# Performance work log

Hardware: AMD Instinct MI355X
Metric: run time of the kernel (lower is better)

Reference implementation:

```python
import jax, jax.numpy as jnp
import numpy as np

N, E, IN_C, DIM, OUT_C, G = 40000, 640000, 128, 128, 16, 256
BN_EPS = 1e-5

def setup_inputs() -> dict:
    key = jax.random.key(0)
    ks = jax.random.split(key, 24)
    x = jax.random.normal(ks[0], (N, IN_C), dtype=jnp.float32)
    edge_index = jax.random.randint(ks[1], (2, E), 0, N, dtype=jnp.int32)
    batch = jnp.sort(jax.random.randint(ks[2], (N,), 0, G, dtype=jnp.int32))
    s = 1.0 / np.sqrt(DIM)
    # layer 1 (in_channels -> dim)
    W1_0 = jax.random.uniform(ks[3], (IN_C, DIM), jnp.float32, -s, s)
    b1_0 = jnp.zeros((DIM,), jnp.float32)
    g_0 = jnp.ones((DIM,), jnp.float32)
    bt_0 = jnp.zeros((DIM,), jnp.float32)
    W2_0 = jax.random.uniform(ks[4], (DIM, DIM), jnp.float32, -s, s)
    b2_0 = jnp.zeros((DIM,), jnp.float32)
    # layers 2-5 stacked (dim -> dim)
    W1s = jax.random.uniform(ks[5], (4, DIM, DIM), jnp.float32, -s, s)
    b1s = jnp.zeros((4, DIM), jnp.float32)
    gs = jnp.ones((4, DIM), jnp.float32)
    bts = jnp.zeros((4, DIM), jnp.float32)
    W2s = jax.random.uniform(ks[6], (4, DIM, DIM), jnp.float32, -s, s)
    b2s = jnp.zeros((4, DIM), jnp.float32)
    lin1_W = jax.random.uniform(ks[7], (DIM, DIM), jnp.float32, -s, s)
    lin1_b = jnp.zeros((DIM,), jnp.float32)
    lin2_W = jax.random.uniform(ks[8], (DIM, OUT_C), jnp.float32, -s, s)
    lin2_b = jnp.zeros((OUT_C,), jnp.float32)
    return dict(x=x, edge_index=edge_index, batch=batch, num_graphs=G,
                W1_0=W1_0, b1_0=b1_0, g_0=g_0, bt_0=bt_0, W2_0=W2_0, b2_0=b2_0,
                W1s=W1s, b1s=b1s, gs=gs, bts=bts, W2s=W2s, b2s=b2s,
                lin1_W=lin1_W, lin1_b=lin1_b, lin2_W=lin2_W, lin2_b=lin2_b)

def _gin_layer(x, src, dst, W1, b1, g, bt, W2, b2):
    # GIN aggregation: (1 + eps) * x_i + sum_{j in N(i)} x_j, eps = 0
    agg = jax.ops.segment_sum(x[src], dst, num_segments=x.shape[0])
    h = (x + agg) @ W1 + b1
    # BatchNorm1d over nodes (training-mode batch stats, biased variance)
    mu = h.mean(axis=0)
    var = h.var(axis=0)
    h = (h - mu) * jax.lax.rsqrt(var + BN_EPS) * g + bt
    h = jax.nn.relu(h)
    return jax.nn.relu(h @ W2 + b2)

def reference(x, edge_index, batch, num_graphs,
              W1_0, b1_0, g_0, bt_0, W2_0, b2_0,
              W1s, b1s, gs, bts, W2s, b2s,
              lin1_W, lin1_b, lin2_W, lin2_b):
    src, dst = edge_index[0], edge_index[1]
    h = _gin_layer(x, src, dst, W1_0, b1_0, g_0, bt_0, W2_0, b2_0)
    for i in range(4):
        h = _gin_layer(h, src, dst, W1s[i], b1s[i], gs[i], bts[i], W2s[i], b2s[i])
    x1 = h  # dropout p=0.2 in eval mode = identity
    pooled = jax.ops.segment_sum(x1, batch, num_segments=num_graphs)  # [G, DIM]
    out = jax.nn.relu(pooled @ lin1_W + lin1_b)
    out = out @ lin2_W + lin2_b
    return (jax.nn.log_softmax(out, axis=-1), x1)
```

## Files before the change

### kernel.cpp

```cpp
#include <hip/hip_runtime.h>

namespace {

constexpr int N    = 40000;
constexpr int E    = 640000;
constexpr int DIM  = 128;
constexpr int NG   = 256;
constexpr int OUTC = 16;
constexpr int STRIDE = 48;
constexpr float BN_EPS = 1e-5f;

typedef __attribute__((ext_vector_type(8))) short bf16x8;
typedef __attribute__((ext_vector_type(4))) float f32x4;
typedef __attribute__((ext_vector_type(2))) float f32x2;

__device__ __forceinline__ void atomAddF(float* p, float v) {
  unsafeAtomicAdd(p, v);
}

__device__ __forceinline__ unsigned b16r(float f) {
  unsigned u = __float_as_uint(f);
  return (u + 0x7fffu + ((u >> 16) & 1u)) >> 16;
}
__device__ __forceinline__ unsigned pack2(float a, float b) {
  return b16r(a) | (b16r(b) << 16);
}

__device__ __forceinline__ unsigned pk4_fp8(float4 v) {
  unsigned u = __builtin_amdgcn_cvt_pk_fp8_f32(v.x, v.y, 0, false);
  u = __builtin_amdgcn_cvt_pk_fp8_f32(v.z, v.w, u, true);
  return u;
}
__device__ __forceinline__ void addfp8x4(float* a, unsigned u) {
  f32x2 lo = __builtin_amdgcn_cvt_pk_f32_fp8(u, false);
  f32x2 hi = __builtin_amdgcn_cvt_pk_f32_fp8(u, true);
  a[0] += lo[0]; a[1] += lo[1]; a[2] += hi[0]; a[3] += hi[1];
}
__device__ __forceinline__ void add16(float* a, const uint4 v) {
  addfp8x4(a, v.x); addfp8x4(a + 4, v.y); addfp8x4(a + 8, v.z); addfp8x4(a + 12, v.w);
}

__device__ __forceinline__ int rot4(int r) {
  return ((r << 1) | ((r >> 3) & 1)) & 15;
}

__device__ __forceinline__ bf16x8 bnrelu8(bf16x8 a, const float* sc, const float* sh) {
  union { bf16x8 v; unsigned u[4]; } in, out;
  in.v = a;
#pragma unroll
  for (int p = 0; p < 4; ++p) {
    float lo = __uint_as_float(in.u[p] << 16);
    float hi = __uint_as_float(in.u[p] & 0xffff0000u);
    lo = fmaxf(fmaf(lo, sc[2 * p], sh[2 * p]), 0.f);
    hi = fmaxf(fmaf(hi, sc[2 * p + 1], sh[2 * p + 1]), 0.f);
    out.u[p] = pack2(lo, hi);
  }
  return out.v;
}

constexpr int CVT_B   = (N * DIM / 4) / 256;
constexpr int FILL_B  = E / 256;
constexpr int TRANS_B = 10 * DIM / 4;

__global__ __launch_bounds__(256) void prep_kernel(const float* __restrict__ x,
                                                   unsigned char* __restrict__ xf8,
                                                   const int* __restrict__ src,
                                                   const int* __restrict__ dst,
                                                   int* __restrict__ cnt,
                                                   int* __restrict__ col,
                                                   const float* __restrict__ W1_0,
                                                   const float* __restrict__ W2_0,
                                                   const float* __restrict__ W1s,
                                                   const float* __restrict__ W2s,
                                                   ushort* __restrict__ Wt) {
  const int b = blockIdx.x;
  if (b < CVT_B) {
    const int i = b * 256 + threadIdx.x;
    float4 v = ((const float4*)x)[i];
    ((unsigned*)xf8)[i] = pk4_fp8(v);
  } else if (b < CVT_B + FILL_B) {
    const int e = (b - CVT_B) * 256 + threadIdx.x;
    const int d = dst[e];
    int p = atomicAdd(&cnt[d], 1);
    if (p < STRIDE) col[d * STRIDE + p] = src[e];
  } else {
    const int ob   = (b - CVT_B - FILL_B) * 4 + (threadIdx.x >> 6);
    const int lane = threadIdx.x & 63;
    const int m = ob >> 7;
    const int c = ob & 127;
    const int l = m >> 1;
    const float* W;
    if (l == 0) W = (m & 1) ? W2_0 : W1_0;
    else        W = ((m & 1) ? W2s : W1s) + (size_t)(l - 1) * DIM * DIM;
    const int k = lane * 2;
    float f0 = W[(size_t)k * DIM + c];
    float f1 = W[(size_t)(k + 1) * DIM + c];
    ((unsigned*)Wt)[((size_t)m * DIM + c) * 64 + lane] = pack2(f0, f1);
  }
}


__global__ __launch_bounds__(256) void gin1_fused(const unsigned char* __restrict__ xf8,
                                                  const int* __restrict__ cnt,
                                                  const int* __restrict__ col,
                                                  const ushort* __restrict__ Wt1,
                                                  const float* __restrict__ b1,
                                                  ushort* __restrict__ h,
                                                  float* __restrict__ stats8) {
  __shared__ uint4 tile4[32 * 16];
  const int tid   = threadIdx.x;
  const int node0 = blockIdx.x * 32;

  {
    const int r = tid >> 3;
    const int l = tid & 7;
    const int node = node0 + r;
    const uint4* __restrict__ x16 = (const uint4*)xf8;
    float a[16];
#pragma unroll
    for (int i = 0; i < 16; ++i) a[i] = 0.f;
    add16(a, x16[(size_t)node * 8 + l]);
    int n = cnt[node];
    n = (n < STRIDE) ? n : STRIDE;
    const int base = node * STRIDE;
    int k = 0;
    for (; k + 4 <= n; k += 4) {
      int j0 = col[base + k], j1 = col[base + k + 1];
      int j2 = col[base + k + 2], j3 = col[base + k + 3];
      uint4 v0 = x16[(size_t)j0 * 8 + l];
      uint4 v1 = x16[(size_t)j1 * 8 + l];
      uint4 v2 = x16[(size_t)j2 * 8 + l];
      uint4 v3 = x16[(size_t)j3 * 8 + l];
      add16(a, v0); add16(a, v1); add16(a, v2); add16(a, v3);
    }
    for (; k < n; ++k) add16(a, x16[(size_t)col[base + k] * 8 + l]);
    uint4 o0 = {pack2(a[0], a[1]), pack2(a[2], a[3]), pack2(a[4], a[5]), pack2(a[6], a[7])};
    uint4 o1 = {pack2(a[8], a[9]), pack2(a[10], a[11]), pack2(a[12], a[13]), pack2(a[14], a[15])};
    const int sw = rot4(r & 15);
    tile4[r * 16 + ((2 * l) ^ sw)]     = o0;
    tile4[r * 16 + ((2 * l + 1) ^ sw)] = o1;
  }
  __syncthreads();

  const int lane = tid & 63;
  const int c0   = __builtin_amdgcn_readfirstlane((tid >> 6) * 32);
  const int lr   = lane & 15;
  const int lg   = lane >> 4;

  const bf16x8* __restrict__ tb = (const bf16x8*)tile4;
  const int r0 = lr, r1 = lr + 16;
  const int sw0 = rot4(lr);

  const ushort* __restrict__ brow = Wt1 + (size_t)(c0 + lr) * DIM + lg * 8;

  f32x4 acc[2][2];
#pragma unroll
  for (int i = 0; i < 2; ++i)
#pragma unroll
    for (int j = 0; j < 2; ++j) acc[i][j] = {0, 0, 0, 0};

#pragma unroll
  for (int ks = 0; ks < 4; ++ks) {
    bf16x8 a0 = tb[r0 * 16 + ((lg + ks * 4) ^ sw0)];
    bf16x8 a1 = tb[r1 * 16 + ((lg + ks * 4) ^ sw0)];
    bf16x8 b0 = *(const bf16x8*)(brow + ks * 32);
    bf16x8 b1v = *(const bf16x8*)(brow + 16 * DIM + ks * 32);
    acc[0][0] = __builtin_amdgcn_mfma_f32_16x16x32_bf16(a0, b0, acc[0][0], 0, 0, 0);
    acc[0][1] = __builtin_amdgcn_mfma_f32_16x16x32_bf16(a0, b1v, acc[0][1], 0, 0, 0);
    acc[1][0] = __builtin_amdgcn_mfma_f32_16x16x32_bf16(a1, b0, acc[1][0], 0, 0, 0);
    acc[1][1] = __builtin_amdgcn_mfma_f32_16x16x32_bf16(a1, b1v, acc[1][1], 0, 0, 0);
  }

  float s[2] = {0, 0}, q[2] = {0, 0};
#pragma unroll
  for (int rf = 0; rf < 2; ++rf) {
#pragma unroll
    for (int cf = 0; cf < 2; ++cf) {
      const int colidx = c0 + cf * 16 + lr;
      const float bb = b1[colidx];
#pragma unroll
      for (int rg = 0; rg < 4; ++rg) {
        float v = acc[rf][cf][rg] + bb;
        const int row = node0 + rf * 16 + lg * 4 + rg;
        __builtin_nontemporal_store((ushort)b16r(v), &h[(size_t)row * DIM + colidx]);
        s[cf] += v; q[cf] = fmaf(v, v, q[cf]);
      }
    }
  }
#pragma unroll
  for (int cf = 0; cf < 2; ++cf) {
    float ss = s[cf], qq = q[cf];
    ss += __shfl_xor(ss, 16); ss += __shfl_xor(ss, 32);
    qq += __shfl_xor(qq, 16); qq += __shfl_xor(qq, 32);
    if (lg == 0) {
      float* st = stats8 + (blockIdx.x & 7) * 2 * DIM;
      atomAddF(&st[c0 + cf * 16 + lr], ss);
      atomAddF(&st[DIM + c0 + cf * 16 + lr], qq);
    }
  }
}


template <int F32OUT>
__global__ __launch_bounds__(256) void gin2_fused(const ushort* __restrict__ h,
                                                  const float* __restrict__ stats8,
                                                  const float* __restrict__ gamma,
                                                  const float* __restrict__ beta,
                                                  const ushort* __restrict__ Wt2,
                                                  const float* __restrict__ b2,
                                                  unsigned char* __restrict__ xf8,
                                                  float* __restrict__ outf) {
  __shared__ float lsc[DIM], lsh[DIM];
  const int tid = threadIdx.x;
  if (tid < DIM) {
    float s = 0.f, q = 0.f;
#pragma unroll
    for (int p = 0; p < 8; ++p) {
      s += stats8[p * 2 * DIM + tid];
      q += stats8[p * 2 * DIM + DIM + tid];
    }
    const float inv_n = 1.0f / N;
    float mu  = s * inv_n;
    float var = q * inv_n - mu * mu;
    float sc  = gamma[tid] * rsqrtf(var + BN_EPS);
    lsc[tid] = sc;
    lsh[tid] = beta[tid] - mu * sc;
  }
  __syncthreads();

  const int lane = tid & 63;
  const int c0   = __builtin_amdgcn_readfirstlane((tid >> 6) * 32);
  const int lr   = lane & 15;
  const int lg   = lane >> 4;
  const int row0 = blockIdx.x * 32;

  const ushort* __restrict__ arow = h + (size_t)(row0 + lr) * DIM + lg * 8;
  const ushort* __restrict__ brow = Wt2 + (size_t)(c0 + lr) * DIM + lg * 8;

  f32x4 acc00 = {0, 0, 0, 0}, acc01 = {0, 0, 0, 0}, acc10 = {0, 0, 0, 0}, acc11 = {0, 0, 0, 0};

#pragma unroll
  for (int ks = 0; ks < 4; ++ks) {
    const int ch0 = lg * 8 + ks * 32;
    float sc[8], sh[8];
    *(float4*)(sc)     = *(const float4*)&lsc[ch0];
    *(float4*)(sc + 4) = *(const float4*)&lsc[ch0 + 4];
    *(float4*)(sh)     = *(const float4*)&lsh[ch0];
    *(float4*)(sh + 4) = *(const float4*)&lsh[ch0 + 4];
    bf16x8 ra0 = __builtin_nontemporal_load((const bf16x8*)(arow + ks * 32));
    bf16x8 ra1 = __builtin_nontemporal_load((const bf16x8*)(arow + 16 * DIM + ks * 32));
    bf16x8 a0 = bnrelu8(ra0, sc, sh);
    bf16x8 a1 = bnrelu8(ra1, sc, sh);
    bf16x8 b0 = *(const bf16x8*)(brow + ks * 32);
    bf16x8 b1 = *(const bf16x8*)(brow + 16 * DIM + ks * 32);
    acc00 = __builtin_amdgcn_mfma_f32_16x16x32_bf16(a0, b0, acc00, 0, 0, 0);
    acc01 = __builtin_amdgcn_mfma_f32_16x16x32_bf16(a0, b1, acc01, 0, 0, 0);
    acc10 = __builtin_amdgcn_mfma_f32_16x16x32_bf16(a1, b0, acc10, 0, 0, 0);
    acc11 = __builtin_amdgcn_mfma_f32_16x16x32_bf16(a1, b1, acc11, 0, 0, 0);
  }

  const float bia0 = b2[c0 + lr];
  const float bia1 = b2[c0 + 16 + lr];
  f32x4 accs[2][2] = {{acc00, acc01}, {acc10, acc11}};
#pragma unroll
  for (int rf = 0; rf < 2; ++rf) {
#pragma unroll
    for (int cf = 0; cf < 2; ++cf) {
      const int colidx = c0 + cf * 16 + lr;
      const float bb = cf ? bia1 : bia0;
#pragma unroll
      for (int rg = 0; rg < 4; ++rg) {
        float v = fmaxf(accs[rf][cf][rg] + bb, 0.f);
        const int row = row0 + rf * 16 + lg * 4 + rg;
        if (F32OUT) {
          __builtin_nontemporal_store(v, &outf[(size_t)row * DIM + colidx]);
        } else {
          float vp = __shfl_xor(v, 1);
          if (!(lr & 1)) {
            unsigned pk = __builtin_amdgcn_cvt_pk_fp8_f32(v, vp, 0, false);
            *(ushort*)(xf8 + (size_t)row * DIM + colidx) = (ushort)pk;
          }
        }
      }
    }
  }
}


__global__ __launch_bounds__(256) void pool_kernel(const float* __restrict__ x1,
                                                   const int* __restrict__ batch,
                                                   float* __restrict__ pooled) {
  const int grp  = (blockIdx.x * blockDim.x + threadIdx.x) >> 5;
  const int lane = threadIdx.x & 31;
  const int node0 = grp * 64;
  if (node0 >= N) return;
  const int end = (node0 + 64 < N) ? (node0 + 64) : N;
  float4 acc = {0, 0, 0, 0};
  int cur = batch[node0];
  for (int n = node0; n < end; ++n) {
    int b = batch[n];
    if (b != cur) {
      atomAddF(&pooled[(size_t)cur * DIM + lane * 4 + 0], acc.x);
      atomAddF(&pooled[(size_t)cur * DIM + lane * 4 + 1], acc.y);
      atomAddF(&pooled[(size_t)cur * DIM + lane * 4 + 2], acc.z);
      atomAddF(&pooled[(size_t)cur * DIM + lane * 4 + 3], acc.w);
      acc = {0, 0, 0, 0};
      cur = b;
    }
    f32x4 v = __builtin_nontemporal_load((const f32x4*)x1 + (size_t)n * 32 + lane);
    acc.x += v[0]; acc.y += v[1]; acc.z += v[2]; acc.w += v[3];
  }
  atomAddF(&pooled[(size_t)cur * DIM + lane * 4 + 0], acc.x);
  atomAddF(&pooled[(size_t)cur * DIM + lane * 4 + 1], acc.y);
  atomAddF(&pooled[(size_t)cur * DIM + lane * 4 + 2], acc.z);
  atomAddF(&pooled[(size_t)cur * DIM + lane * 4 + 3], acc.w);
}


__global__ __launch_bounds__(128) void mlp_kernel(const float* __restrict__ pooled,
                                                  const float* __restrict__ W1,
                                                  const float* __restrict__ b1,
                                                  const float* __restrict__ W2,
                                                  const float* __restrict__ b2,
                                                  float* __restrict__ out) {
  const int gidx = blockIdx.x;
  const int t    = threadIdx.x;
  __shared__ float p[DIM], a1[DIM];
  p[t] = pooled[(size_t)gidx * DIM + t];
  __syncthreads();
  float acc = b1[t];
  for (int k = 0; k < DIM; ++k) acc = fmaf(p[k], W1[(size_t)k * DIM + t], acc);
  a1[t] = fmaxf(acc, 0.f);
  __syncthreads();
  if (t < OUTC) {
    float o = b2[t];
    for (int k = 0; k < DIM; ++k) o = fmaf(a1[k], W2[(size_t)k * OUTC + t], o);
    float m = o;
    for (int s = 8; s >= 1; s >>= 1) m = fmaxf(m, __shfl_xor(m, s, 16));
    float e = __expf(o - m);
    float se = e;
    for (int s = 8; s >= 1; s >>= 1) se += __shfl_xor(se, s, 16);
    out[(size_t)gidx * OUTC + t] = o - m - __logf(se);
  }
}

}

extern "C" void kernel_launch(void* const* d_in, const int* in_sizes, int n_in,
                              void* d_out, int out_size, void* d_ws, size_t ws_size,
                              hipStream_t stream) {
  const float* x     = (const float*)d_in[0];
  const int*   ei    = (const int*)d_in[1];
  const int*   batch = (const int*)d_in[2];
  const float* W1_0  = (const float*)d_in[4];
  const float* b1_0  = (const float*)d_in[5];
  const float* g_0   = (const float*)d_in[6];
  const float* bt_0  = (const float*)d_in[7];
  const float* W2_0  = (const float*)d_in[8];
  const float* b2_0  = (const float*)d_in[9];
  const float* W1s   = (const float*)d_in[10];
  const float* b1s   = (const float*)d_in[11];
  const float* gs    = (const float*)d_in[12];
  const float* bts   = (const float*)d_in[13];
  const float* W2s   = (const float*)d_in[14];
  const float* b2s   = (const float*)d_in[15];
  const float* lin1W = (const float*)d_in[16];
  const float* lin1b = (const float*)d_in[17];
  const float* lin2W = (const float*)d_in[18];
  const float* lin2b = (const float*)d_in[19];

  float* out_ls = (float*)d_out;
  float* x1_out = (float*)d_out + NG * OUTC;

  char* w = (char*)d_ws;
  auto alloc = [&](size_t bytes) -> void* {
    void* p = (void*)w;
    w += (bytes + 255) & ~(size_t)255;
    return p;
  };
  int*    cnt      = (int*)alloc((size_t)N * 4);
  float*  statsAll = (float*)alloc((size_t)(5 * 8 * 2 * DIM + NG * DIM) * 4);
  float*  pooled   = statsAll + 5 * 8 * 2 * DIM;
  const size_t zero_bytes = (size_t)((N * 4 + 255) & ~255) +
                            (size_t)(5 * 8 * 2 * DIM + NG * DIM) * 4;

  int*    col    = (int*)alloc((size_t)N * STRIDE * 4);
  unsigned char* xf8 = (unsigned char*)alloc((size_t)N * DIM);
  ushort* act    = (ushort*)alloc((size_t)N * DIM * 2);
  ushort* Wt     = (ushort*)alloc((size_t)10 * DIM * DIM * 2);

  const int* src = ei;
  const int* dst = ei + E;

  (void)hipMemsetAsync(cnt, 0, zero_bytes, stream);

  prep_kernel<<<CVT_B + FILL_B + TRANS_B, 256, 0, stream>>>(x, xf8, src, dst, cnt, col,
                                                            W1_0, W2_0, W1s, W2s, Wt);

  for (int l = 0; l < 5; ++l) {
    const float* b1 = (l == 0) ? b1_0 : b1s + (size_t)(l - 1) * DIM;
    const float* gg = (l == 0) ? g_0  : gs  + (size_t)(l - 1) * DIM;
    const float* bb = (l == 0) ? bt_0 : bts + (size_t)(l - 1) * DIM;
    const float* b2 = (l == 0) ? b2_0 : b2s + (size_t)(l - 1) * DIM;
    const ushort* Wt1 = Wt + (size_t)(2 * l) * DIM * DIM;
    const ushort* Wt2 = Wt + (size_t)(2 * l + 1) * DIM * DIM;
    float* stats8 = statsAll + (size_t)l * 8 * 2 * DIM;

    gin1_fused<<<N / 32, 256, 0, stream>>>(xf8, cnt, col, Wt1, b1, act, stats8);
    if (l == 4)
      gin2_fused<1><<<N / 32, 256, 0, stream>>>(act, stats8, gg, bb, Wt2, b2, nullptr, x1_out);
    else
      gin2_fused<0><<<N / 32, 256, 0, stream>>>(act, stats8, gg, bb, Wt2, b2, xf8, nullptr);
  }

  {
    int groups = (N + 63) / 64;
    int blocks = (groups * 32 + 255) / 256;
    pool_kernel<<<blocks, 256, 0, stream>>>(x1_out, batch, pooled);
  }
  mlp_kernel<<<NG, 128, 0, stream>>>(pooled, lin1W, lin1b, lin2W, lin2b, out_ls);
}
```

Measured before the change: 321.7 us.

## Fuse graph pooling into last GIN layer, compact CSR indices, drop memset

Removes the separate pool kernel by doing segmented per-graph sums with atomics in the epilogue of the final gin2 kernel, so x1 is not read back. Replaces hipMemsetAsync with zeroing blocks inside prep_kernel and splits the CSR fill into its own kernel, which is needed because zeroing must finish before the count atomics. Column indices are stored as ushort to halve adjacency traffic. Nontemporal hints on the h store and load are dropped so the intermediate can stay in cache. Risks: ushort indices only hold values below 65536 (N=40000 fits), more atomics on pooled, and one extra kernel launch.

```diff
diff --git a/kernel.cpp b/kernel.cpp
--- a/kernel.cpp
+++ b/kernel.cpp
@@ -59,32 +59,27 @@
 }
 
 constexpr int CVT_B   = (N * DIM / 4) / 256;
-constexpr int FILL_B  = E / 256;
 constexpr int TRANS_B = 10 * DIM / 4;
+constexpr size_t ZERO_BYTES = (size_t)((N * 4 + 255) & ~255) +
+                              (size_t)(5 * 8 * 2 * DIM) * 4 +
+                              (size_t)(NG * DIM) * 4;
+constexpr int ZERO_B  = (int)((ZERO_BYTES / 16 + 255) / 256);
 
 __global__ __launch_bounds__(256) void prep_kernel(const float* __restrict__ x,
                                                    unsigned char* __restrict__ xf8,
-                                                   const int* __restrict__ src,
-                                                   const int* __restrict__ dst,
-                                                   int* __restrict__ cnt,
-                                                   int* __restrict__ col,
                                                    const float* __restrict__ W1_0,
                                                    const float* __restrict__ W2_0,
                                                    const float* __restrict__ W1s,
                                                    const float* __restrict__ W2s,
-                                                   ushort* __restrict__ Wt) {
+                                                   ushort* __restrict__ Wt,
+                                                   uint4* __restrict__ zp) {
   const int b = blockIdx.x;
   if (b < CVT_B) {
     const int i = b * 256 + threadIdx.x;
     float4 v = ((const float4*)x)[i];
     ((unsigned*)xf8)[i] = pk4_fp8(v);
-  } else if (b < CVT_B + FILL_B) {
-    const int e = (b - CVT_B) * 256 + threadIdx.x;
-    const int d = dst[e];
-    int p = atomicAdd(&cnt[d], 1);
-    if (p < STRIDE) col[d * STRIDE + p] = src[e];
-  } else {
-    const int ob   = (b - CVT_B - FILL_B) * 4 + (threadIdx.x >> 6);
+  } else if (b < CVT_B + TRANS_B) {
+    const int ob   = (b - CVT_B) * 4 + (threadIdx.x >> 6);
     const int lane = threadIdx.x & 63;
     const int m = ob >> 7;
     const int c = ob & 127;
@@ -96,13 +91,27 @@
     float f0 = W[(size_t)k * DIM + c];
     float f1 = W[(size_t)(k + 1) * DIM + c];
     ((unsigned*)Wt)[((size_t)m * DIM + c) * 64 + lane] = pack2(f0, f1);
-  }
+  } else {
+    const size_t i = (size_t)(b - CVT_B - TRANS_B) * 256 + threadIdx.x;
+    if (i * 16 < ZERO_BYTES) zp[i] = {0, 0, 0, 0};
+  }
+}
+
+
+__global__ __launch_bounds__(256) void fill_kernel(const int* __restrict__ src,
+                                                   const int* __restrict__ dst,
+                                                   int* __restrict__ cnt,
+                                                   ushort* __restrict__ col) {
+  const int e = blockIdx.x * 256 + threadIdx.x;
+  const int d = dst[e];
+  int p = atomicAdd(&cnt[d], 1);
+  if (p < STRIDE) col[d * STRIDE + p] = (ushort)src[e];
 }
 
 
 __global__ __launch_bounds__(256) void gin1_fused(const unsigned char* __restrict__ xf8,
                                                   const int* __restrict__ cnt,
-                                                  const int* __restrict__ col,
+                                                  const ushort* __restrict__ col,
                                                   const ushort* __restrict__ Wt1,
                                                   const float* __restrict__ b1,
                                                   ushort* __restrict__ h,
@@ -182,7 +191,7 @@
       for (int rg = 0; rg < 4; ++rg) {
         float v = acc[rf][cf][rg] + bb;
         const int row = node0 + rf * 16 + lg * 4 + rg;
-        __builtin_nontemporal_store((ushort)b16r(v), &h[(size_t)row * DIM + colidx]);
+        h[(size_t)row * DIM + colidx] = (ushort)b16r(v);
         s[cf] += v; q[cf] = fmaf(v, v, q[cf]);
       }
     }
@@ -209,7 +218,9 @@
                                                   const ushort* __restrict__ Wt2,
                                                   const float* __restrict__ b2,
                                                   unsigned char* __restrict__ xf8,
-                                                  float* __restrict__ outf) {
+                                                  float* __restrict__ outf,
+                                                  const int* __restrict__ batch,
+                                                  float* __restrict__ pooled) {
   __shared__ float lsc[DIM], lsh[DIM];
   const int tid = threadIdx.x;
   if (tid < DIM) {
@@ -247,10 +258,8 @@
     *(float4*)(sc + 4) = *(const float4*)&lsc[ch0 + 4];
     *(float4*)(sh)     = *(const float4*)&lsh[ch0];
     *(float4*)(sh + 4) = *(const float4*)&lsh[ch0 + 4];
-    bf16x8 ra0 = __builtin_nontemporal_load((const bf16x8*)(arow + ks * 32));
-    bf16x8 ra1 = __builtin_nontemporal_load((const bf16x8*)(arow + 16 * DIM + ks * 32));
-    bf16x8 a0 = bnrelu8(ra0, sc, sh);
-    bf16x8 a1 = bnrelu8(ra1, sc, sh);
+    bf16x8 a0 = bnrelu8(*(const bf16x8*)(arow + ks * 32), sc, sh);
+    bf16x8 a1 = bnrelu8(*(const bf16x8*)(arow + 16 * DIM + ks * 32), sc, sh);
     bf16x8 b0 = *(const bf16x8*)(brow + ks * 32);
     bf16x8 b1 = *(const bf16x8*)(brow + 16 * DIM + ks * 32);
     acc00 = __builtin_amdgcn_mfma_f32_16x16x32_bf16(a0, b0, acc00, 0, 0, 0);
@@ -262,19 +271,44 @@
   const float bia0 = b2[c0 + lr];
   const float bia1 = b2[c0 + 16 + lr];
   f32x4 accs[2][2] = {{acc00, acc01}, {acc10, acc11}};
-#pragma unroll
-  for (int rf = 0; rf < 2; ++rf) {
-#pragma unroll
-    for (int cf = 0; cf < 2; ++cf) {
-      const int colidx = c0 + cf * 16 + lr;
-      const float bb = cf ? bia1 : bia0;
-#pragma unroll
-      for (int rg = 0; rg < 4; ++rg) {
-        float v = fmaxf(accs[rf][cf][rg] + bb, 0.f);
-        const int row = row0 + rf * 16 + lg * 4 + rg;
-        if (F32OUT) {
-          __builtin_nontemporal_store(v, &outf[(size_t)row * DIM + colidx]);
-        } else {
+
+  if (F32OUT) {
+    const int rbase = row0 + lg * 4;
+#pragma unroll
+    for (int rf = 0; rf < 2; ++rf) {
+      const int r0_ = rbase + rf * 16;
+      int4 b4 = *(const int4*)&batch[r0_];
+      const int bb_[4] = {b4.x, b4.y, b4.z, b4.w};
+#pragma unroll
+      for (int cf = 0; cf < 2; ++cf) {
+        const int colidx = c0 + cf * 16 + lr;
+        const float bia = cf ? bia1 : bia0;
+        float run = 0.f;
+        int cur = bb_[0];
+#pragma unroll
+        for (int rg = 0; rg < 4; ++rg) {
+          float v = fmaxf(accs[rf][cf][rg] + bia, 0.f);
+          __builtin_nontemporal_store(v, &outf[(size_t)(r0_ + rg) * DIM + colidx]);
+          if (bb_[rg] != cur) {
+            atomAddF(&pooled[(size_t)cur * DIM + colidx], run);
+            run = 0.f; cur = bb_[rg];
+          }
+          run += v;
+        }
+        atomAddF(&pooled[(size_t)cur * DIM + colidx], run);
+      }
+    }
+  } else {
+#pragma unroll
+    for (int rf = 0; rf < 2; ++rf) {
+#pragma unroll
+      for (int cf = 0; cf < 2; ++cf) {
+        const int colidx = c0 + cf * 16 + lr;
+        const float bia = cf ? bia1 : bia0;
+#pragma unroll
+        for (int rg = 0; rg < 4; ++rg) {
+          float v = fmaxf(accs[rf][cf][rg] + bia, 0.f);
+          const int row = row0 + rf * 16 + lg * 4 + rg;
           float vp = __shfl_xor(v, 1);
           if (!(lr & 1)) {
             unsigned pk = __builtin_amdgcn_cvt_pk_fp8_f32(v, vp, 0, false);
@@ -284,36 +318,6 @@
       }
     }
   }
-}
-
-
-__global__ __launch_bounds__(256) void pool_kernel(const float* __restrict__ x1,
-                                                   const int* __restrict__ batch,
-                                                   float* __restrict__ pooled) {
-  const int grp  = (blockIdx.x * blockDim.x + threadIdx.x) >> 5;
-  const int lane = threadIdx.x & 31;
-  const int node0 = grp * 64;
-  if (node0 >= N) return;
-  const int end = (node0 + 64 < N) ? (node0 + 64) : N;
-  float4 acc = {0, 0, 0, 0};
-  int cur = batch[node0];
-  for (int n = node0; n < end; ++n) {
-    int b = batch[n];
-    if (b != cur) {
-      atomAddF(&pooled[(size_t)cur * DIM + lane * 4 + 0], acc.x);
-      atomAddF(&pooled[(size_t)cur * DIM + lane * 4 + 1], acc.y);
-      atomAddF(&pooled[(size_t)cur * DIM + lane * 4 + 2], acc.z);
-      atomAddF(&pooled[(size_t)cur * DIM + lane * 4 + 3], acc.w);
-      acc = {0, 0, 0, 0};
-      cur = b;
-    }
-    f32x4 v = __builtin_nontemporal_load((const f32x4*)x1 + (size_t)n * 32 + lane);
-    acc.x += v[0]; acc.y += v[1]; acc.z += v[2]; acc.w += v[3];
-  }
-  atomAddF(&pooled[(size_t)cur * DIM + lane * 4 + 0], acc.x);
-  atomAddF(&pooled[(size_t)cur * DIM + lane * 4 + 1], acc.y);
-  atomAddF(&pooled[(size_t)cur * DIM + lane * 4 + 2], acc.z);
-  atomAddF(&pooled[(size_t)cur * DIM + lane * 4 + 3], acc.w);
 }
 
 
@@ -379,12 +383,10 @@
     return p;
   };
   int*    cnt      = (int*)alloc((size_t)N * 4);
-  float*  statsAll = (float*)alloc((size_t)(5 * 8 * 2 * DIM + NG * DIM) * 4);
-  float*  pooled   = statsAll + 5 * 8 * 2 * DIM;
-  const size_t zero_bytes = (size_t)((N * 4 + 255) & ~255) +
-                            (size_t)(5 * 8 * 2 * DIM + NG * DIM) * 4;
-
-  int*    col    = (int*)alloc((size_t)N * STRIDE * 4);
+  float*  statsAll = (float*)alloc((size_t)(5 * 8 * 2 * DIM) * 4);
+  float*  pooled   = (float*)alloc((size_t)NG * DIM * 4);
+
+  ushort* col    = (ushort*)alloc((size_t)N * STRIDE * 2);
   unsigned char* xf8 = (unsigned char*)alloc((size_t)N * DIM);
   ushort* act    = (ushort*)alloc((size_t)N * DIM * 2);
   ushort* Wt     = (ushort*)alloc((size_t)10 * DIM * DIM * 2);
@@ -392,10 +394,9 @@
   const int* src = ei;
   const int* dst = ei + E;
 
-  (void)hipMemsetAsync(cnt, 0, zero_bytes, stream);
-
-  prep_kernel<<<CVT_B + FILL_B + TRANS_B, 256, 0, stream>>>(x, xf8, src, dst, cnt, col,
-                                                            W1_0, W2_0, W1s, W2s, Wt);
+  prep_kernel<<<CVT_B + TRANS_B + ZERO_B, 256, 0, stream>>>(x, xf8, W1_0, W2_0, W1s, W2s,
+                                                            Wt, (uint4*)cnt);
+  fill_kernel<<<E / 256, 256, 0, stream>>>(src, dst, cnt, col);
 
   for (int l = 0; l < 5; ++l) {
     const float* b1 = (l == 0) ? b1_0 : b1s + (size_t)(l - 1) * DIM;
@@ -408,15 +409,12 @@
 
     gin1_fused<<<N / 32, 256, 0, stream>>>(xf8, cnt, col, Wt1, b1, act, stats8);
     if (l == 4)
-      gin2_fused<1><<<N / 32, 256, 0, stream>>>(act, stats8, gg, bb, Wt2, b2, nullptr, x1_out);
+      gin2_fused<1><<<N / 32, 256, 0, stream>>>(act, stats8, gg, bb, Wt2, b2, nullptr,
+                                                x1_out, batch, pooled);
     else
-      gin2_fused<0><<<N / 32, 256, 0, stream>>>(act, stats8, gg, bb, Wt2, b2, xf8, nullptr);
-  }
-
-  {
-    int groups = (N + 63) / 64;
-    int blocks = (groups * 32 + 255) / 256;
-    pool_kernel<<<blocks, 256, 0, stream>>>(x1_out, batch, pooled);
-  }
+      gin2_fused<0><<<N / 32, 256, 0, stream>>>(act, stats8, gg, bb, Wt2, b2, xf8,
+                                                nullptr, nullptr, nullptr);
+  }
+
   mlp_kernel<<<NG, 128, 0, stream>>>(pooled, lin1W, lin1b, lin2W, lin2b, out_ls);
 }
```

Result: faster. 262.0 us (median of 2 runs) (-18.6%).
